# Optimization experiments

Measured on AMD Instinct MI355X. Metric: run time of the kernel, lower is better.

## Reference

```python
import jax, jax.numpy as jnp
import numpy as np
import math

B, S, D, H = 8, 1024, 512, 8  # batch, seqlen, d_model, heads
DK = D // H

def setup_inputs() -> dict:
    key = jax.random.key(0)
    ks = jax.random.split(key, 8)
    std = 1.0 / math.sqrt(D)
    return {
        "x": jax.random.normal(ks[0], (B, S, D), jnp.float32),
        "utT_similarities": jax.random.uniform(ks[1], (B, S, S), jnp.float32),
        "Wk": jax.random.normal(ks[2], (D, D), jnp.float32) * std,
        "bk": jnp.zeros((D,), jnp.float32),
        "Wv": jax.random.normal(ks[3], (D, D), jnp.float32) * std,
        "bv": jnp.zeros((D,), jnp.float32),
        "Wo": jax.random.normal(ks[4], (D, D), jnp.float32) * std,
        "bo": jnp.zeros((D,), jnp.float32),
        "gammas": jax.random.normal(ks[5], (H, 1, 1), jnp.float32) * 0.1,
    }

def reference(x, utT_similarities, Wk, bk, Wv, bv, Wo, bo, gammas):
    b, s, d = x.shape
    h = gammas.shape[0]
    dk = d // h
    NEG = -1e32

    def split_heads(t):  # [b,s,d] -> [b,h,s,dk]
        return t.reshape(b, s, h, dk).transpose(0, 2, 1, 3)

    # kq_same=True: q and k share k_linear
    q = split_heads(x @ Wk.T + bk)
    k = q
    v = split_heads(x @ Wv.T + bv)

    scores = jnp.einsum('bhid,bhjd->bhij', q, k) / jnp.sqrt(jnp.float32(dk))
    scores = scores * utT_similarities[:, None, :, :]

    mask = jnp.tril(jnp.ones((s, s), dtype=bool))  # causal, incl diagonal (mask=1)

    # distance-decay block (no_grad in torch -> stop_gradient)
    s_ = jax.nn.softmax(jnp.where(mask, scores, NEG), axis=-1) * mask
    distcum = jnp.cumsum(s_, axis=-1)
    disttotal = jnp.sum(s_, axis=-1, keepdims=True)
    idx = jnp.arange(s)
    position_effect = jnp.abs(idx[None, :] - idx[:, None]).astype(jnp.float32)  # [s,s]
    dist_scores = jnp.sqrt(jnp.clip((disttotal - distcum) * position_effect, 0.0, None))
    dist_scores = jax.lax.stop_gradient(dist_scores)

    gamma = -jax.nn.softplus(gammas)[None]  # [1,h,1,1]
    total_effect = jnp.clip(jnp.exp(dist_scores * gamma), 1e-5, 1e5)

    scores = jax.nn.softmax(jnp.where(mask, scores * total_effect, NEG), axis=-1)
    # zero_pad=False (mask=1 path), dropout is identity in eval
    out = jnp.einsum('bhij,bhjd->bhid', scores, v)
    out = out.transpose(0, 2, 1, 3).reshape(b, s, d)
    return out @ Wo.T + bo
```

## Files before the change

### kernel.cpp

```cpp
#include <hip/hip_runtime.h>
#include <math.h>

#define NB   8
#define SS   1024
#define DD   512
#define HH   8
#define DKK  64
#define NEGF (-3.0e38f)
#define SC   (0.125f * 1.4426950408889634f)

#define QSTR 88
#define SSTR 257
#define PSTR 280

typedef _Float16 half8 __attribute__((ext_vector_type(8)));
typedef float    f32x4 __attribute__((ext_vector_type(4)));

#define GLDS16(g, l) __builtin_amdgcn_global_load_lds( \
    (const __attribute__((address_space(1))) void*)(g), \
    (__attribute__((address_space(3))) void*)(l), 16, 0, 0)

template<int CTRL, int RM, int BM, bool BC>
__device__ __forceinline__ float dpp_f(float x) {
    return __builtin_bit_cast(float,
        __builtin_amdgcn_update_dpp(0, __builtin_bit_cast(int, x),
                                    CTRL, RM, BM, BC));
}

__device__ __forceinline__ float scan64(float x) {
    x += dpp_f<0x111, 0xf, 0xf, true >(x);
    x += dpp_f<0x112, 0xf, 0xf, true >(x);
    x += dpp_f<0x114, 0xf, 0xf, true >(x);
    x += dpp_f<0x118, 0xf, 0xf, true >(x);
    x += dpp_f<0x142, 0xa, 0xf, false>(x);
    x += dpp_f<0x143, 0xc, 0xf, false>(x);
    return x;
}

__device__ __forceinline__ float redsum64(float x) {
    x += dpp_f<0xB1,  0xf, 0xf, true>(x);
    x += dpp_f<0x4E,  0xf, 0xf, true>(x);
    x += dpp_f<0x141, 0xf, 0xf, true>(x);
    x += dpp_f<0x140, 0xf, 0xf, true>(x);
    x += __shfl_xor(x, 16);
    x += __shfl_xor(x, 32);
    return x;
}

__device__ __forceinline__ float bcast63(float x) {
    return __builtin_bit_cast(float,
        __builtin_amdgcn_readlane(__builtin_bit_cast(int, x), 63));
}

__global__ __launch_bounds__(256) void cvt_fp16(
    const float* __restrict__ x,  _Float16* __restrict__ xh,
    const float* __restrict__ wk, _Float16* __restrict__ wkh,
    const float* __restrict__ wv, _Float16* __restrict__ wvh,
    const float* __restrict__ wo, _Float16* __restrict__ woh)
{
    const size_t NX = (size_t)NB * SS * DD;
    const size_t NW = (size_t)DD * DD;
    size_t f = ((size_t)blockIdx.x * 256 + threadIdx.x) * 8;
    const float* src; _Float16* dst; size_t off;
    if (f < NX)               { src = x;  dst = xh;  off = f; }
    else if (f < NX + NW)     { src = wk; dst = wkh; off = f - NX; }
    else if (f < NX + 2*NW)   { src = wv; dst = wvh; off = f - NX - 2*NW + NW; }
    else                      { src = wo; dst = woh; off = f - NX - 2*NW; }
    float4 f0 = *(const float4*)&src[off];
    float4 f1 = *(const float4*)&src[off + 4];
    half8 hv = {(_Float16)f0.x,(_Float16)f0.y,(_Float16)f0.z,(_Float16)f0.w,
                (_Float16)f1.x,(_Float16)f1.y,(_Float16)f1.z,(_Float16)f1.w};
    *(half8*)&dst[off] = hv;
}

__global__ __launch_bounds__(256) void gemm_qv(
    const _Float16* __restrict__ xh,
    const _Float16* __restrict__ wkh, const float* __restrict__ bk,
    const _Float16* __restrict__ wvh, const float* __restrict__ bv,
    _Float16* __restrict__ q_ws, _Float16* __restrict__ vt_ws)
{
    __shared__ __align__(16) _Float16 Ah[128 * 32];
    __shared__ __align__(16) _Float16 Bh[128 * 32];

    const int m0  = blockIdx.x * 128;
    const int n0c = blockIdx.y * 128;
    const bool is_v = (n0c >= DD);
    const _Float16* __restrict__ Wp = is_v ? wvh : wkh;
    const float*    __restrict__ bp = is_v ? bv : bk;
    const int n0 = n0c & (DD - 1);

    const int tid  = threadIdx.x;
    const int w    = tid >> 6;
    const int lane = tid & 63;
    const int quad = lane >> 4;
    const int n    = lane & 15;
    const int wm   = w >> 1, wn = w & 1;

    const int ci0 = (w * 2 + 0) * 64 + lane;
    const int ci1 = (w * 2 + 1) * 64 + lane;
    const int r0c = ci0 >> 2, c0c = (ci0 & 3) * 8;
    const int r1c = ci1 >> 2, c1c = (ci1 & 3) * 8;
    _Float16* ldsA0 = &Ah[(w * 2 + 0) * 512];
    _Float16* ldsA1 = &Ah[(w * 2 + 1) * 512];
    _Float16* ldsB0 = &Bh[(w * 2 + 0) * 512];
    _Float16* ldsB1 = &Bh[(w * 2 + 1) * 512];

    f32x4 acc[4][4] = {};

    for (int k0 = 0; k0 < DD; k0 += 32) {
        __syncthreads();
        GLDS16(&xh[(size_t)(m0 + r0c) * DD + k0 + c0c], ldsA0);
        GLDS16(&xh[(size_t)(m0 + r1c) * DD + k0 + c1c], ldsA1);
        GLDS16(&Wp[(size_t)(n0 + r0c) * DD + k0 + c0c], ldsB0);
        GLDS16(&Wp[(size_t)(n0 + r1c) * DD + k0 + c1c], ldsB1);
        __syncthreads();
        half8 af[4], bf[4];
        #pragma unroll
        for (int mi = 0; mi < 4; ++mi)
            af[mi] = *(const half8*)&Ah[(wm*64 + mi*16 + n) * 32 + quad*8];
        #pragma unroll
        for (int ni = 0; ni < 4; ++ni)
            bf[ni] = *(const half8*)&Bh[(wn*64 + ni*16 + n) * 32 + quad*8];
        #pragma unroll
        for (int mi = 0; mi < 4; ++mi)
            #pragma unroll
            for (int ni = 0; ni < 4; ++ni)
                acc[mi][ni] = __builtin_amdgcn_mfma_f32_16x16x32_f16(
                    af[mi], bf[ni], acc[mi][ni], 0, 0, 0);
    }

    #pragma unroll
    for (int mi = 0; mi < 4; ++mi) {
        #pragma unroll
        for (int ni = 0; ni < 4; ++ni) {
            const int col = n0 + wn*64 + ni*16 + n;
            const int h   = col >> 6;
            const int dk  = col & 63;
            const float bias = bp[col];
            const int gbase = m0 + wm*64 + mi*16 + quad*4;
            const int bidx  = gbase >> 10;
            const int sr    = gbase & (SS - 1);
            if (!is_v) {
                #pragma unroll
                for (int reg = 0; reg < 4; ++reg)
                    q_ws[((size_t)(bidx * HH + h) * SS + sr + reg) * DKK + dk] =
                        (_Float16)(acc[mi][ni][reg] + bias);
            } else {
                _Float16 h4[4];
                #pragma unroll
                for (int reg = 0; reg < 4; ++reg)
                    h4[reg] = (_Float16)(acc[mi][ni][reg] + bias);
                *(uint2*)&vt_ws[((size_t)(bidx * HH + h) * DKK + dk) * SS + sr] =
                    *(uint2*)h4;
            }
        }
    }
}

__global__ __launch_bounds__(256) void gemm_out(
    const _Float16* __restrict__ A,
    const _Float16* __restrict__ woh, const float* __restrict__ bo,
    float* __restrict__ out)
{
    __shared__ __align__(16) _Float16 Ah[128 * 32];
    __shared__ __align__(16) _Float16 Bh[128 * 32];

    const int m0 = blockIdx.x * 128;
    const int n0 = blockIdx.y * 128;

    const int tid  = threadIdx.x;
    const int w    = tid >> 6;
    const int lane = tid & 63;
    const int quad = lane >> 4;
    const int n    = lane & 15;
    const int wm   = w >> 1, wn = w & 1;

    const int ci0 = (w * 2 + 0) * 64 + lane;
    const int ci1 = (w * 2 + 1) * 64 + lane;
    const int r0c = ci0 >> 2, c0c = (ci0 & 3) * 8;
    const int r1c = ci1 >> 2, c1c = (ci1 & 3) * 8;
    _Float16* ldsA0 = &Ah[(w * 2 + 0) * 512];
    _Float16* ldsA1 = &Ah[(w * 2 + 1) * 512];
    _Float16* ldsB0 = &Bh[(w * 2 + 0) * 512];
    _Float16* ldsB1 = &Bh[(w * 2 + 1) * 512];

    f32x4 acc[4][4] = {};

    for (int k0 = 0; k0 < DD; k0 += 32) {
        __syncthreads();
        GLDS16(&A[(size_t)(m0 + r0c) * DD + k0 + c0c], ldsA0);
        GLDS16(&A[(size_t)(m0 + r1c) * DD + k0 + c1c], ldsA1);
        GLDS16(&woh[(size_t)(n0 + r0c) * DD + k0 + c0c], ldsB0);
        GLDS16(&woh[(size_t)(n0 + r1c) * DD + k0 + c1c], ldsB1);
        __syncthreads();
        half8 af[4], bf[4];
        #pragma unroll
        for (int mi = 0; mi < 4; ++mi)
            af[mi] = *(const half8*)&Ah[(wm*64 + mi*16 + n) * 32 + quad*8];
        #pragma unroll
        for (int ni = 0; ni < 4; ++ni)
            bf[ni] = *(const half8*)&Bh[(wn*64 + ni*16 + n) * 32 + quad*8];
        #pragma unroll
        for (int mi = 0; mi < 4; ++mi)
            #pragma unroll
            for (int ni = 0; ni < 4; ++ni)
                acc[mi][ni] = __builtin_amdgcn_mfma_f32_16x16x32_f16(
                    af[mi], bf[ni], acc[mi][ni], 0, 0, 0);
    }

    #pragma unroll
    for (int mi = 0; mi < 4; ++mi) {
        #pragma unroll
        for (int ni = 0; ni < 4; ++ni) {
            const int col  = n0 + wn*64 + ni*16 + n;
            const float bias = bo[col];
            const int gbase = m0 + wm*64 + mi*16 + quad*4;
            #pragma unroll
            for (int reg = 0; reg < 4; ++reg)
                out[(size_t)(gbase + reg) * DD + col] = acc[mi][ni][reg] + bias;
        }
    }
}

__global__ __launch_bounds__(1024) void attn_mfma(
    const _Float16* __restrict__ q,
    const _Float16* __restrict__ vt,
    const float* __restrict__ utT,
    const float* __restrict__ gammas,
    _Float16* __restrict__ attn)
{
    __shared__ __align__(16) unsigned char smem[4 * 16 * SSTR * 4];
    __shared__ __align__(16) _Float16 q_lds[16 * QSTR];
    float*    s_lds = (float*)smem;
    _Float16* p_lds = (_Float16*)smem;

    const int tid  = threadIdx.x;
    const int w    = tid >> 6;
    const int lane = tid & 63;
    const int quad = lane >> 4;
    const int n    = lane & 15;
    const int bh   = blockIdx.y;
    const int b    = bh >> 3;
    const int h    = bh & 7;
    const int r0   = ((SS / 16 - 1) - blockIdx.x) * 16;

    const _Float16* __restrict__ kq  = q  + (size_t)bh * SS * DKK;
    const _Float16* __restrict__ vtp = vt + (size_t)bh * DKK * SS;

    const int nchunk = (r0 + 16 + 255) >> 8;
    const int nt     = nchunk * 4;

    if (tid < 256) {
        const int row = tid >> 4;
        const int c   = tid & 15;
        *(uint2*)&q_lds[row * QSTR + c * 4] =
            *(const uint2*)&kq[(size_t)(r0 + row) * DKK + c * 4];
    }
    __syncthreads();

    float sreg[16];
    #pragma unroll
    for (int t2 = 0; t2 < 16; ++t2) sreg[t2] = NEGF;

    #pragma unroll
    for (int c0 = 0; c0 < 4; ++c0) {
        if (c0 < nchunk) {
            const int j0  = c0 * 256;
            const int buf = c0 * 16 * SSTR;
            const int jbase = j0 + w * 16;
            if (jbase <= r0 + 15) {
                const _Float16* krow = &kq[(size_t)(jbase + n) * DKK];
                half8 b0 = *(const half8*)&krow[quad * 8];
                half8 b1 = *(const half8*)&krow[32 + quad * 8];
                half8 a0 = *(const half8*)&q_lds[n * QSTR + quad * 8];
                half8 a1 = *(const half8*)&q_lds[n * QSTR + 32 + quad * 8];
                f32x4 d = {0.f, 0.f, 0.f, 0.f};
                d = __builtin_amdgcn_mfma_f32_16x16x32_f16(a0, b0, d, 0, 0, 0);
                d = __builtin_amdgcn_mfma_f32_16x16x32_f16(a1, b1, d, 0, 0, 0);
                const int j = jbase + n;
                #pragma unroll
                for (int reg = 0; reg < 4; ++reg) {
                    const int i = r0 + quad * 4 + reg;
                    float val = NEGF;
                    if (j <= i)
                        val = d[reg] * SC * utT[((size_t)b * SS + i) * SS + j];
                    s_lds[buf + (quad * 4 + reg) * SSTR + w * 16 + n] = val;
                }
            } else {
                #pragma unroll
                for (int reg = 0; reg < 4; ++reg)
                    s_lds[buf + (quad * 4 + reg) * SSTR + w * 16 + n] = NEGF;
            }
        }
    }
    __syncthreads();

    #pragma unroll
    for (int c0 = 0; c0 < 4; ++c0) {
        if (c0 < nchunk) {
            const int buf = c0 * 16 * SSTR;
            #pragma unroll
            for (int ttl = 0; ttl < 4; ++ttl)
                sreg[c0 * 4 + ttl] = s_lds[buf + w * SSTR + ttl * 64 + lane];
        }
    }

    const int i_row = r0 + w;
    const int ntw_u = (i_row >> 6) + 1;
    const int ntw   = (nt < ntw_u) ? nt : ntw_u;

    float cs[16];
    float carry = 0.f;
    #pragma unroll
    for (int t2 = 0; t2 < 16; ++t2) {
        if (t2 < ntw) {
            const float e  = __builtin_amdgcn_exp2f(sreg[t2]);
            const float xv = scan64(e);
            cs[t2] = carry + xv;
            carry += bcast63(xv);
        }
    }
    const float z1     = carry;
    const float inv_z1 = 1.0f / z1;

    const float g     = gammas[h];
    const float gl2   = -log1pf(__expf(g)) * 1.4426950408889634f;
    const float flane = (float)lane;

    float z2 = 0.f;
    #pragma unroll
    for (int t2 = 0; t2 < 16; ++t2) {
        if (t2 < ntw) {
            const float pe = (float)(i_row - t2 * 64) - flane;
            const float dd = fmaxf((z1 - cs[t2]) * pe, 0.0f) * inv_z1;
            float te = __builtin_amdgcn_exp2f(__builtin_amdgcn_sqrtf(dd) * gl2);
            te = fmaxf(te, 1e-5f);
            const float p = __builtin_amdgcn_exp2f(sreg[t2] * te);
            sreg[t2] = p;
            z2 += p;
        } else {
            sreg[t2] = 0.f;
        }
    }
    z2 = redsum64(z2);
    const float inv_z2 = 1.0f / z2;

    __syncthreads();

    #pragma unroll
    for (int c0 = 0; c0 < 4; ++c0) {
        if (c0 < nchunk) {
            #pragma unroll
            for (int ttl = 0; ttl < 4; ++ttl)
                p_lds[c0 * 16 * PSTR + w * PSTR + ttl * 64 + lane] =
                    (_Float16)(sreg[c0 * 4 + ttl] * inv_z2);
        }
    }

    const int KT = (r0 + 16 + 31) >> 5;
    const _Float16* vrow = &vtp[(size_t)(w * 16 + n) * SS];
    half8 vb[4] = {};
    if (w < 4) {
        #pragma unroll
        for (int u = 0; u < 4; ++u)
            if (u < KT) vb[u] = *(const half8*)&vrow[u * 32 + quad * 8];
    }
    __syncthreads();

    f32x4 oacc = {0.f, 0.f, 0.f, 0.f};
    if (w < 4) {
        for (int kt0 = 0; kt0 < KT; kt0 += 4) {
            half8 cur[4];
            #pragma unroll
            for (int u = 0; u < 4; ++u) cur[u] = vb[u];
            #pragma unroll
            for (int u = 0; u < 4; ++u) {
                const int k = kt0 + 4 + u;
                if (k < KT) vb[u] = *(const half8*)&vrow[k * 32 + quad * 8];
            }
            #pragma unroll
            for (int u = 0; u < 4; ++u) {
                const int k = kt0 + u;
                if (k < KT) {
                    half8 a = *(const half8*)&p_lds[((k >> 3) * 16 + n) * PSTR +
                                                    (k & 7) * 32 + quad * 8];
                    oacc = __builtin_amdgcn_mfma_f32_16x16x32_f16(
                        a, cur[u], oacc, 0, 0, 0);
                }
            }
        }
        #pragma unroll
        for (int reg = 0; reg < 4; ++reg) {
            const int i = r0 + quad * 4 + reg;
            attn[(((size_t)b * SS + i) * HH + h) * DKK + w * 16 + n] =
                (_Float16)oacc[reg];
        }
    }
}

extern "C" void kernel_launch(void* const* d_in, const int* in_sizes, int n_in,
                              void* d_out, int out_size, void* d_ws, size_t ws_size,
                              hipStream_t stream) {
    const float* x      = (const float*)d_in[0];
    const float* utT    = (const float*)d_in[1];
    const float* Wk     = (const float*)d_in[2];
    const float* bk     = (const float*)d_in[3];
    const float* Wv     = (const float*)d_in[4];
    const float* bv     = (const float*)d_in[5];
    const float* Wo     = (const float*)d_in[6];
    const float* bo     = (const float*)d_in[7];
    const float* gammas = (const float*)d_in[8];
    float* out = (float*)d_out;

    const size_t NX  = (size_t)NB * SS * DD;
    const size_t NW  = (size_t)DD * DD;
    const size_t per = NX;

    _Float16* p      = (_Float16*)d_ws;
    _Float16* xh     = p;  p += NX;
    _Float16* wkh    = p;  p += NW;
    _Float16* wvh    = p;  p += NW;
    _Float16* woh    = p;  p += NW;
    _Float16* q_ws   = p;  p += per;
    _Float16* vt_ws  = p;  p += per;
    _Float16* attn_h = p;  p += per;

    const int cvt_blocks = (int)((NX + 3 * NW) / 8 / 256);
    cvt_fp16<<<cvt_blocks, dim3(256), 0, stream>>>(
        x, xh, Wk, wkh, Wv, wvh, Wo, woh);

    dim3 g1(64, 8);
    gemm_qv<<<g1, dim3(256), 0, stream>>>(xh, wkh, bk, wvh, bv, q_ws, vt_ws);

    dim3 g2(SS / 16, NB * HH);
    attn_mfma<<<g2, dim3(1024), 0, stream>>>(q_ws, vt_ws, utT, gammas, attn_h);

    dim3 g3(64, 4);
    gemm_out<<<g3, dim3(256), 0, stream>>>(attn_h, woh, bo, out);
}
```

Measured before the change: 334.0 us.

## Swap MFMA operands to transpose scores, load Q to registers, XOR-swizzle LDS

The Q tile is now loaded straight from global memory into registers instead of being staged through LDS, which removes one __syncthreads and the q_lds buffer. The MFMA operands are swapped so each lane holds four consecutive columns of one row. That allows a single float4 load of the utT similarity row and a single float4 store into the score buffer. The padded LDS stride is replaced with an XOR swizzle to avoid bank conflicts while keeping 16-byte aligned vector stores. The risk is that the swizzle must be matched exactly on the read side, and any unchanged later code that uses the old score layout would break.

```diff
diff --git a/kernel.cpp b/kernel.cpp
--- a/kernel.cpp
+++ b/kernel.cpp
@@ -9,8 +9,7 @@
 #define NEGF (-3.0e38f)
 #define SC   (0.125f * 1.4426950408889634f)
 
-#define QSTR 88
-#define SSTR 257
+#define SCHUNK (16 * 256)
 #define PSTR 280
 
 typedef _Float16 half8 __attribute__((ext_vector_type(8)));
@@ -229,8 +228,7 @@
     const float* __restrict__ gammas,
     _Float16* __restrict__ attn)
 {
-    __shared__ __align__(16) unsigned char smem[4 * 16 * SSTR * 4];
-    __shared__ __align__(16) _Float16 q_lds[16 * QSTR];
+    __shared__ __align__(16) unsigned char smem[4 * SCHUNK * 4];
     float*    s_lds = (float*)smem;
     _Float16* p_lds = (_Float16*)smem;
 
@@ -249,59 +247,49 @@
 
     const int nchunk = (r0 + 16 + 255) >> 8;
     const int nt     = nchunk * 4;
-
-    if (tid < 256) {
-        const int row = tid >> 4;
-        const int c   = tid & 15;
-        *(uint2*)&q_lds[row * QSTR + c * 4] =
-            *(const uint2*)&kq[(size_t)(r0 + row) * DKK + c * 4];
-    }
-    __syncthreads();
-
-    float sreg[16];
-    #pragma unroll
-    for (int t2 = 0; t2 < 16; ++t2) sreg[t2] = NEGF;
+    const int i_lane = r0 + n;
+
+    const half8 qa0 = *(const half8*)&kq[(size_t)(r0 + n) * DKK + quad * 8];
+    const half8 qa1 = *(const half8*)&kq[(size_t)(r0 + n) * DKK + 32 + quad * 8];
+
+    const float* __restrict__ utrow = &utT[((size_t)b * SS + i_lane) * SS];
+    const int scol = (w * 16 + quad * 4) ^ ((n & 7) << 2);
 
     #pragma unroll
     for (int c0 = 0; c0 < 4; ++c0) {
         if (c0 < nchunk) {
-            const int j0  = c0 * 256;
-            const int buf = c0 * 16 * SSTR;
-            const int jbase = j0 + w * 16;
+            const int jbase = c0 * 256 + w * 16;
+            f32x4 v;
             if (jbase <= r0 + 15) {
                 const _Float16* krow = &kq[(size_t)(jbase + n) * DKK];
-                half8 b0 = *(const half8*)&krow[quad * 8];
-                half8 b1 = *(const half8*)&krow[32 + quad * 8];
-                half8 a0 = *(const half8*)&q_lds[n * QSTR + quad * 8];
-                half8 a1 = *(const half8*)&q_lds[n * QSTR + 32 + quad * 8];
+                half8 k0 = *(const half8*)&krow[quad * 8];
+                half8 k1 = *(const half8*)&krow[32 + quad * 8];
+                f32x4 ut = *(const f32x4*)&utrow[jbase + quad * 4];
                 f32x4 d = {0.f, 0.f, 0.f, 0.f};
-                d = __builtin_amdgcn_mfma_f32_16x16x32_f16(a0, b0, d, 0, 0, 0);
-                d = __builtin_amdgcn_mfma_f32_16x16x32_f16(a1, b1, d, 0, 0, 0);
-                const int j = jbase + n;
+                d = __builtin_amdgcn_mfma_f32_16x16x32_f16(k0, qa0, d, 0, 0, 0);
+                d = __builtin_amdgcn_mfma_f32_16x16x32_f16(k1, qa1, d, 0, 0, 0);
                 #pragma unroll
                 for (int reg = 0; reg < 4; ++reg) {
-                    const int i = r0 + quad * 4 + reg;
-                    float val = NEGF;
-                    if (j <= i)
-                        val = d[reg] * SC * utT[((size_t)b * SS + i) * SS + j];
-                    s_lds[buf + (quad * 4 + reg) * SSTR + w * 16 + n] = val;
+                    const int j = jbase + quad * 4 + reg;
+                    v[reg] = (j <= i_lane) ? d[reg] * SC * ut[reg] : NEGF;
                 }
             } else {
-                #pragma unroll
-                for (int reg = 0; reg < 4; ++reg)
-                    s_lds[buf + (quad * 4 + reg) * SSTR + w * 16 + n] = NEGF;
+                v = (f32x4){NEGF, NEGF, NEGF, NEGF};
             }
+            *(f32x4*)&s_lds[c0 * SCHUNK + n * 256 + scol] = v;
         }
     }
     __syncthreads();
 
+    float sreg[16];
+    const int pcol = lane ^ ((w & 7) << 2);
     #pragma unroll
     for (int c0 = 0; c0 < 4; ++c0) {
         if (c0 < nchunk) {
-            const int buf = c0 * 16 * SSTR;
             #pragma unroll
             for (int ttl = 0; ttl < 4; ++ttl)
-                sreg[c0 * 4 + ttl] = s_lds[buf + w * SSTR + ttl * 64 + lane];
+                sreg[c0 * 4 + ttl] =
+                    s_lds[c0 * SCHUNK + w * 256 + ttl * 64 + pcol];
         }
     }
 
```

Result: no change. 334.2 us (+0.1%).
